# Kernel optimization log

Hardware: AMD Instinct MI355X
Metric: run time of the kernel (lower is better)

The kernel has to match this reference:

```python
import jax, jax.numpy as jnp
import numpy as np

EMBED_DIM = 512
NUM_HEADS = 8
HEAD_DIM = EMBED_DIM // NUM_HEADS
REL_MAX = 16
NUM_POS_IDS = 2 * REL_MAX + 1 + 1  # 34 (directed + padding id)
PADDING_IDX = 0
B, S = 2, 2048


def setup_inputs() -> dict:
    key = jax.random.key(0)
    ks = jax.random.split(key, 9)
    Q = jax.random.normal(ks[0], (B, S, EMBED_DIM), dtype=jnp.float32)
    K = jax.random.normal(ks[1], (B, S, EMBED_DIM), dtype=jnp.float32)
    V = jax.random.normal(ks[2], (B, S, EMBED_DIM), dtype=jnp.float32)
    rel_pos_ids = jax.random.randint(ks[3], (B, S, S), 0, NUM_POS_IDS, dtype=jnp.int64) if jax.config.jax_enable_x64 else jax.random.randint(ks[3], (B, S, S), 0, NUM_POS_IDS, dtype=jnp.int32)
    scale = 0.02
    Wq = jax.random.normal(ks[4], (EMBED_DIM, EMBED_DIM), dtype=jnp.float32) * scale
    Wk = jax.random.normal(ks[5], (EMBED_DIM, EMBED_DIM), dtype=jnp.float32) * scale
    Wv = jax.random.normal(ks[6], (EMBED_DIM, EMBED_DIM), dtype=jnp.float32) * scale
    Wo = jax.random.normal(ks[7], (EMBED_DIM, EMBED_DIM), dtype=jnp.float32) * scale
    rel_emb = jax.random.normal(ks[8], (NUM_POS_IDS, EMBED_DIM), dtype=jnp.float32) * scale
    rel_emb = rel_emb.at[PADDING_IDX].set(0.0)  # nn.Embedding padding_idx row is zero
    return {"Q": Q, "K": K, "V": V, "rel_pos_ids": rel_pos_ids,
            "Wq": Wq, "Wk": Wk, "Wv": Wv, "Wo": Wo, "rel_emb": rel_emb}


def _proj(x, W):
    # Linear (no bias) then strided head split: view(B, S, head_dim, H) -> (B, H, S, head_dim)
    b, s, _ = x.shape
    y = x @ W.T
    return y.reshape(b, s, HEAD_DIM, NUM_HEADS).transpose(0, 3, 1, 2)


def _forward(Q, K, V, rel_pos_ids, Wq, Wk, Wv, Wo, rel_emb):
    b, sq, _ = Q.shape
    Qp = _proj(Q, Wq)  # (B, H, Sq, hd)
    Kp = _proj(K, Wk)  # (B, H, Sk, hd)
    Vp = _proj(V, Wv)  # (B, H, Sk, hd)

    # rel_embeds split per head with the same strided layout: (P, hd, H) -> (H, P, hd)
    R = rel_emb.reshape(NUM_POS_IDS, HEAD_DIM, NUM_HEADS).transpose(2, 0, 1)
    # Q_rel: (B, H, Sq, P)
    Q_rel = jnp.einsum('bhsd,hpd->bhsp', Qp, R)
    # gather per-pair relative bias: (B, H, Sq, Sk)
    rel_shift = jnp.take_along_axis(Q_rel, rel_pos_ids[:, None, :, :], axis=3)
    mask = (rel_pos_ids == PADDING_IDX)[:, None, :, :]
    rel_shift = jnp.where(mask, -jnp.inf, rel_shift)

    energy = (jnp.einsum('bhqd,bhkd->bhqk', Qp, Kp) + rel_shift) / jnp.sqrt(jnp.float32(HEAD_DIM))
    attn = jax.nn.softmax(energy, axis=-1)
    out = jnp.einsum('bhqk,bhkd->bhqd', attn, Vp)  # (B, H, Sq, hd)
    # inverse of strided split: (B, Sq, hd, H) -> flatten last two
    out = out.transpose(0, 2, 3, 1).reshape(b, sq, EMBED_DIM)
    return out @ Wo.T


def reference(Q, K, V, rel_pos_ids, Wq, Wk, Wv, Wo, rel_emb):
    return _forward(Q, K, V, rel_pos_ids, Wq, Wk, Wv, Wo, rel_emb)
```

## Files before the change

kernel.cpp:

```cpp
#include <hip/hip_runtime.h>
#include <cstdint>
#include <cstddef>

#define SEQ   2048
#define BBAT  2
#define EMBED 512
#define NH    8
#define HD    64
#define NPOS  34

typedef __bf16 bf16;
typedef __bf16 bf16x8 __attribute__((ext_vector_type(8)));
typedef float  f32x4  __attribute__((ext_vector_type(4)));
typedef int    int32x4 __attribute__((ext_vector_type(4)));

#define ESCALE 0.1803368801111204f

__device__ __forceinline__ f32x4 mfma16(bf16x8 a, bf16x8 b, f32x4 c){
  return __builtin_amdgcn_mfma_f32_16x16x32_bf16(a, b, c, 0, 0, 0);
}

__device__ __forceinline__ void barrier_lgkm(){
  asm volatile("s_waitcnt lgkmcnt(0)" ::: "memory");
  __builtin_amdgcn_s_barrier();
  __builtin_amdgcn_sched_barrier(0);
}

__global__ __launch_bounds__(256) void k_prep(
    const float* __restrict__ Q, const float* __restrict__ K, const float* __restrict__ V,
    const float* __restrict__ Wq, const float* __restrict__ Wk,
    const float* __restrict__ Wv, const float* __restrict__ Wo,
    const float* __restrict__ RE,
    bf16* __restrict__ Qb, bf16* __restrict__ Kb, bf16* __restrict__ Vb,
    bf16* __restrict__ Wall, bf16* __restrict__ Rb)
{
  const int NCONV = 3*524288;
  const int NW = 196608, NO = 262144;
  int i = blockIdx.x*256 + threadIdx.x;
  if (i < NCONV){
    int tsel = i >> 19, j = i & 524287;
    const float* s = tsel==0 ? Q : (tsel==1 ? K : V);
    bf16* d       = tsel==0 ? Qb : (tsel==1 ? Kb : Vb);
    float4 v = ((const float4*)s)[j];
    union { bf16 e[4]; ushort4 u; } pk;
    pk.e[0]=(bf16)v.x; pk.e[1]=(bf16)v.y; pk.e[2]=(bf16)v.z; pk.e[3]=(bf16)v.w;
    ((ushort4*)d)[j] = pk.u;
  } else {
    int j = i - NCONV;
    if (j < NW){
      int w  = j >> 16;
      int r  = j & 65535;
      int np = r >> 7, c4 = (r & 127) << 2;
      const float* W = (w==0) ? Wq : ((w==1) ? Wk : Wv);
      int src = ((np & 63) << 3) + (np >> 6);
      float4 v = *(const float4*)(W + (size_t)src*512 + c4);
      union { bf16 e[4]; ushort4 u; } pk;
      pk.e[0]=(bf16)v.x; pk.e[1]=(bf16)v.y; pk.e[2]=(bf16)v.z; pk.e[3]=(bf16)v.w;
      *(ushort4*)(Wall + (size_t)w*262144 + (size_t)np*512 + c4) = pk.u;
    } else if (j < NW + NO){
      int jj = j - NW;
      int n = jj >> 9, kp = jj & 511;
      int src = ((kp & 63) << 3) + (kp >> 6);
      Wall[(size_t)3*262144 + (size_t)n*512 + kp] = (bf16)Wo[(size_t)n*512 + src];
    } else {
      int jj = j - NW - NO;
      if (jj < 8*48*64){
        int h  = jj / (48*64);
        int r2 = jj - h*(48*64);
        int p  = r2 >> 6, dd = r2 & 63;
        float v = (p < NPOS) ? RE[(size_t)p*512 + dd*8 + h] : 0.f;
        Rb[jj] = (bf16)v;
      }
    }
  }
}

__global__ __launch_bounds__(256,2) void k_gemm_proj(
    const bf16* __restrict__ Qb, const bf16* __restrict__ Kb, const bf16* __restrict__ Vb,
    const bf16* __restrict__ W,  bf16* __restrict__ Qp, bf16* __restrict__ Kp, bf16* __restrict__ Vt)
{
  const bf16* A  = blockIdx.z==0 ? Qb : (blockIdx.z==1 ? Kb : Vb);
  const bf16* Bw = W + (size_t)blockIdx.z*262144;

  __shared__ __align__(16) bf16 As[128][72];
  __shared__ __align__(16) bf16 Bs[64][72];
  const int t = threadIdx.x;
  const int w = t >> 6, lane = t & 63, l15 = lane & 15, quad = lane >> 4;
  const int wm = (w & 1) * 64, wn = (w >> 1) * 32;
  const int m0 = blockIdx.y * 128, n0 = blockIdx.x * 64;

  f32x4 acc[4][2];
  #pragma unroll
  for (int mt=0; mt<4; ++mt)
    #pragma unroll
    for (int nt=0; nt<2; ++nt) acc[mt][nt] = (f32x4){0.f,0.f,0.f,0.f};

  for (int kt = 0; kt < 512; kt += 64){
    #pragma unroll
    for (int i = 0; i < 4; ++i){
      int lin = t + 256*i;
      int r = lin >> 3, c8 = (lin & 7) << 3;
      *(uint4*)&As[r][c8] = *(const uint4*)(A + (size_t)(m0 + r)*512 + kt + c8);
    }
    #pragma unroll
    for (int i = 0; i < 2; ++i){
      int lin = t + 256*i;
      int r = lin >> 3, c8 = (lin & 7) << 3;
      *(uint4*)&Bs[r][c8] = *(const uint4*)(Bw + (size_t)(n0 + r)*512 + kt + c8);
    }
    __syncthreads();
    #pragma unroll
    for (int ks = 0; ks < 2; ++ks){
      bf16x8 am[4], bn[2];
      #pragma unroll
      for (int x=0;x<4;++x) am[x] = *(const bf16x8*)&As[wm + x*16 + l15][ks*32 + quad*8];
      #pragma unroll
      for (int y=0;y<2;++y) bn[y] = *(const bf16x8*)&Bs[wn + y*16 + l15][ks*32 + quad*8];
      #pragma unroll
      for (int mt=0;mt<4;++mt)
        #pragma unroll
        for (int nt=0;nt<2;++nt)
          acc[mt][nt] = mfma16(am[mt], bn[nt], acc[mt][nt]);
    }
    __syncthreads();
  }

  if (blockIdx.z != 2){
    bf16* C = blockIdx.z==0 ? Qp : Kp;
    const float scl = (blockIdx.z==0) ? ESCALE : 1.0f;
    #pragma unroll
    for (int mt=0;mt<4;++mt)
      #pragma unroll
      for (int r=0;r<4;++r){
        int m = m0 + wm + mt*16 + quad*4 + r;
        #pragma unroll
        for (int nt=0;nt<2;++nt)
          C[(size_t)m*512 + n0 + wn + nt*16 + l15] = (bf16)(acc[mt][nt][r] * scl);
      }
  } else {
    bf16 (*VT)[136] = (bf16(*)[136])As;
    #pragma unroll
    for (int mt=0;mt<4;++mt)
      #pragma unroll
      for (int r=0;r<4;++r){
        int m = wm + mt*16 + quad*4 + r;
        #pragma unroll
        for (int nt=0;nt<2;++nt)
          VT[wn + nt*16 + l15][m] = (bf16)acc[mt][nt][r];
      }
    __syncthreads();
    const int h = blockIdx.x, b = m0 >> 11, s0 = m0 & 2047;
    const int n = t >> 2, c0 = (t & 3) * 32;
    bf16* dst = Vt + ((size_t)((b*NH + h)*HD + n))*SEQ + s0 + c0;
    #pragma unroll
    for (int i = 0; i < 4; ++i)
      *(uint4*)(dst + i*8) = *(const uint4*)&VT[n][c0 + i*8];
  }
}

__global__ __launch_bounds__(256,2) void k_gemm_out(
    const bf16* __restrict__ A, const bf16* __restrict__ Bw, float* __restrict__ C)
{
  __shared__ __align__(16) bf16 As[64][72];
  __shared__ __align__(16) bf16 Bs[64][72];
  const int t = threadIdx.x;
  const int w = t >> 6, lane = t & 63, l15 = lane & 15, quad = lane >> 4;
  const int wm = (w & 1) * 32, wn = (w >> 1) * 32;
  const int m0 = blockIdx.y * 64, n0 = blockIdx.x * 64;

  f32x4 acc[2][2];
  #pragma unroll
  for (int mt=0; mt<2; ++mt)
    #pragma unroll
    for (int nt=0; nt<2; ++nt) acc[mt][nt] = (f32x4){0.f,0.f,0.f,0.f};

  for (int kt = 0; kt < 512; kt += 64){
    #pragma unroll
    for (int i = 0; i < 2; ++i){
      int lin = t + 256*i;
      int r = lin >> 3, c8 = (lin & 7) << 3;
      *(uint4*)&As[r][c8] = *(const uint4*)(A  + (size_t)(m0 + r)*512 + kt + c8);
      *(uint4*)&Bs[r][c8] = *(const uint4*)(Bw + (size_t)(n0 + r)*512 + kt + c8);
    }
    __syncthreads();
    #pragma unroll
    for (int ks = 0; ks < 2; ++ks){
      bf16x8 am[2], bn[2];
      #pragma unroll
      for (int x=0;x<2;++x) am[x] = *(const bf16x8*)&As[wm + x*16 + l15][ks*32 + quad*8];
      #pragma unroll
      for (int y=0;y<2;++y) bn[y] = *(const bf16x8*)&Bs[wn + y*16 + l15][ks*32 + quad*8];
      #pragma unroll
      for (int mt=0;mt<2;++mt)
        #pragma unroll
        for (int nt=0;nt<2;++nt)
          acc[mt][nt] = mfma16(am[mt], bn[nt], acc[mt][nt]);
    }
    __syncthreads();
  }
  #pragma unroll
  for (int mt=0;mt<2;++mt)
    #pragma unroll
    for (int r=0;r<4;++r){
      int m = m0 + wm + mt*16 + quad*4 + r;
      #pragma unroll
      for (int nt=0;nt<2;++nt)
        C[(size_t)m*512 + n0 + wn + nt*16 + l15] = acc[mt][nt][r];
    }
}

__global__ __launch_bounds__(256,2) void k_attn(
    const bf16* __restrict__ Qp, const bf16* __restrict__ Kp,
    const bf16* __restrict__ Vt, const bf16* __restrict__ Rb,
    const int* __restrict__ ids, bf16* __restrict__ Out)
{
  __shared__ __align__(16) bf16 Ks[128][72];
  __shared__ __align__(16) bf16 Vs[64][136];
  __shared__ __align__(16) bf16 Ps[64][136];
  __shared__ float lutT[35][65];
  __shared__ float lsum_s[128];

  const int t = threadIdx.x;
  const int b = blockIdx.z, h = blockIdx.y;
  const int q0 = blockIdx.x * 64;
  const int w = t >> 6, lane = t & 63, l15 = lane & 15, quad = lane >> 4;
  const int qh = w & 1, kh = w >> 1;

  const size_t idb = (size_t)b*SEQ*SEQ;
  const bf16* kbase = Kp + (size_t)b*SEQ*EMBED + h*HD;
  const bf16* vbase = Vt + (size_t)(b*NH + h)*HD*SEQ;

  const int krow = t >> 3, kcol = (t & 7) << 3;
  const int vrow = t >> 4, vcol = (t & 15) << 3;

  uint4 ka0, ka1, ka2, ka3, va0, va1, va2, va3;
  uint4 kb0, kb1, kb2, kb3, vb0, vb1, vb2, vb3;
  ka0 = *(const uint4*)(kbase + (size_t)(krow     )*EMBED + kcol);
  ka1 = *(const uint4*)(kbase + (size_t)(krow + 32)*EMBED + kcol);
  ka2 = *(const uint4*)(kbase + (size_t)(krow + 64)*EMBED + kcol);
  ka3 = *(const uint4*)(kbase + (size_t)(krow + 96)*EMBED + kcol);
  va0 = *(const uint4*)(vbase + (size_t)(vrow     )*SEQ + vcol);
  va1 = *(const uint4*)(vbase + (size_t)(vrow + 16)*SEQ + vcol);
  va2 = *(const uint4*)(vbase + (size_t)(vrow + 32)*SEQ + vcol);
  va3 = *(const uint4*)(vbase + (size_t)(vrow + 48)*SEQ + vcol);

  int32x4 nid[2][4];
  #pragma unroll
  for (int mt=0; mt<2; ++mt)
    #pragma unroll
    for (int nt=0; nt<4; ++nt)
      nid[mt][nt] = *(const int32x4*)(ids + idb
          + (size_t)(q0 + qh*32 + mt*16 + l15)*SEQ
          + kh*64 + nt*16 + quad*4);

  {
    const bf16* qbrow = Qp + (size_t)(b*SEQ + q0 + w*16 + l15)*EMBED + h*HD;
    bf16x8 ab0 = *(const bf16x8*)(qbrow + quad*8);
    bf16x8 ab1 = *(const bf16x8*)(qbrow + 32 + quad*8);
    const bf16* rh = Rb + h*3072;
    #pragma unroll
    for (int nt = 0; nt < 3; ++nt){
      bf16x8 r0 = *(const bf16x8*)(rh + (nt*16 + l15)*64 + quad*8);
      bf16x8 r1 = *(const bf16x8*)(rh + (nt*16 + l15)*64 + 32 + quad*8);
      f32x4 c = (f32x4){0.f,0.f,0.f,0.f};
      c = mfma16(ab0, r0, c);
      c = mfma16(ab1, r1, c);
      int p = nt*16 + l15;
      if (p < NPOS){
        #pragma unroll
        for (int r = 0; r < 4; ++r)
          lutT[p][w*16 + quad*4 + r] = (p == 0) ? -1e30f : c[r];
      }
    }
  }

  bf16x8 bq[2][2];
  #pragma unroll
  for (int mt = 0; mt < 2; ++mt){
    const bf16* qrow = Qp + (size_t)(b*SEQ + q0 + qh*32 + mt*16 + l15)*EMBED + h*HD;
    bq[mt][0] = *(const bf16x8*)(qrow + quad*8);
    bq[mt][1] = *(const bf16x8*)(qrow + 32 + quad*8);
  }

  f32x4 acc[2][4];
  #pragma unroll
  for (int mt=0;mt<2;++mt)
    #pragma unroll
    for (int nt=0;nt<4;++nt) acc[mt][nt] = (f32x4){0.f,0.f,0.f,0.f};
  float lsum[2] = {0.f, 0.f};

#define ATTN_BODY(KT, K0,K1,K2,K3, V0,V1,V2,V3, L0,L1,L2,L3, M0,M1,M2,M3)       \
  {                                                                             \
    barrier_lgkm();              \
    *(uint4*)&Ks[krow     ][kcol] = K0;                                         \
    *(uint4*)&Ks[krow + 32][kcol] = K1;                                         \
    *(uint4*)&Ks[krow + 64][kcol] = K2;                                         \
    *(uint4*)&Ks[krow + 96][kcol] = K3;                                         \
    *(uint4*)&Vs[vrow     ][vcol] = V0;                                         \
    *(uint4*)&Vs[vrow + 16][vcol] = V1;                                         \
    *(uint4*)&Vs[vrow + 32][vcol] = V2;                                         \
    *(uint4*)&Vs[vrow + 48][vcol] = V3;                                         \
    if ((KT) < 15){                                                             \
      const bf16* kp2 = kbase + (size_t)(((KT)+1)*128)*EMBED + kcol;            \
      const bf16* vp2 = vbase + ((KT)+1)*128 + vcol;                            \
      L0 = *(const uint4*)(kp2 + (size_t)(krow     )*EMBED);                    \
      L1 = *(const uint4*)(kp2 + (size_t)(krow + 32)*EMBED);                    \
      L2 = *(const uint4*)(kp2 + (size_t)(krow + 64)*EMBED);                    \
      L3 = *(const uint4*)(kp2 + (size_t)(krow + 96)*EMBED);                    \
      M0 = *(const uint4*)(vp2 + (size_t)(vrow     )*SEQ);                      \
      M1 = *(const uint4*)(vp2 + (size_t)(vrow + 16)*SEQ);                      \
      M2 = *(const uint4*)(vp2 + (size_t)(vrow + 32)*SEQ);                      \
      M3 = *(const uint4*)(vp2 + (size_t)(vrow + 48)*SEQ);                      \
    }                                                                           \
    barrier_lgkm();                \
    float wvv[2][4][4];                                                         \
    _Pragma("unroll")                                                           \
    for (int mt = 0; mt < 2; ++mt){                                             \
      const float* lcol = &lutT[0][qh*32 + mt*16 + l15];                        \
      _Pragma("unroll")                                                         \
      for (int nt = 0; nt < 4; ++nt){                                           \
        int32x4 v = nid[mt][nt];                                                \
        wvv[mt][nt][0] = lcol[v[0] * 65];                                       \
        wvv[mt][nt][1] = lcol[v[1] * 65];                                       \
        wvv[mt][nt][2] = lcol[v[2] * 65];                                       \
        wvv[mt][nt][3] = lcol[v[3] * 65];                                       \
      }                                                                         \
    }                                                                           \
    if ((KT) < 15){                                                             \
      _Pragma("unroll")                                                         \
      for (int mt = 0; mt < 2; ++mt)                                            \
        _Pragma("unroll")                                                       \
        for (int nt = 0; nt < 4; ++nt)                                          \
          nid[mt][nt] = *(const int32x4*)(ids + idb                             \
              + (size_t)(q0 + qh*32 + mt*16 + l15)*SEQ                          \
              + (((KT)+1)*128) + kh*64 + nt*16 + quad*4);                       \
    }                                                                           \
    f32x4 sf[2][4];                                                             \
    __builtin_amdgcn_s_setprio(1);                                              \
    _Pragma("unroll")                                                           \
    for (int nt = 0; nt < 4; ++nt){                                             \
      bf16x8 ak0 = *(const bf16x8*)&Ks[kh*64 + nt*16 + l15][quad*8];            \
      bf16x8 ak1 = *(const bf16x8*)&Ks[kh*64 + nt*16 + l15][32 + quad*8];       \
      _Pragma("unroll")                                                         \
      for (int mt = 0; mt < 2; ++mt){                                           \
        f32x4 c = (f32x4){0.f,0.f,0.f,0.f};                                     \
        c = mfma16(ak0, bq[mt][0], c);                                          \
        c = mfma16(ak1, bq[mt][1], c);                                          \
        sf[mt][nt] = c;                                                         \
      }                                                                         \
    }                                                                           \
    __builtin_amdgcn_s_setprio(0);                                              \
    _Pragma("unroll")                                                           \
    for (int mt = 0; mt < 2; ++mt){                                             \
      _Pragma("unroll")                                                         \
      for (int nt = 0; nt < 4; ++nt){                                           \
        union { bf16 e[4]; uint2 u; } pk;                                       \
        float p0 = __builtin_amdgcn_exp2f(sf[mt][nt][0] + wvv[mt][nt][0]);      \
        float p1 = __builtin_amdgcn_exp2f(sf[mt][nt][1] + wvv[mt][nt][1]);      \
        float p2 = __builtin_amdgcn_exp2f(sf[mt][nt][2] + wvv[mt][nt][2]);      \
        float p3 = __builtin_amdgcn_exp2f(sf[mt][nt][3] + wvv[mt][nt][3]);      \
        pk.e[0] = (bf16)p0; pk.e[1] = (bf16)p1;                                 \
        pk.e[2] = (bf16)p2; pk.e[3] = (bf16)p3;                                 \
        lsum[mt] += (p0 + p1) + (p2 + p3);                                      \
        *(uint2*)&Ps[qh*32 + mt*16 + l15][kh*64 + nt*16 + quad*4] = pk.u;       \
      }                                                                         \
    }                                                                           \
    __builtin_amdgcn_s_setprio(1);                                              \
    _Pragma("unroll")                                                           \
    for (int ks = 0; ks < 2; ++ks){                                             \
      bf16x8 ap[2];                                                             \
      _Pragma("unroll")                                                         \
      for (int mt = 0; mt < 2; ++mt)                                            \
        ap[mt] = *(const bf16x8*)&Ps[qh*32 + mt*16 + l15][kh*64 + ks*32 + quad*8]; \
      _Pragma("unroll")                                                         \
      for (int nt = 0; nt < 4; ++nt){                                           \
        bf16x8 bv = *(const bf16x8*)&Vs[nt*16 + l15][kh*64 + ks*32 + quad*8];   \
        _Pragma("unroll")                                                       \
        for (int mt = 0; mt < 2; ++mt)                                          \
          acc[mt][nt] = mfma16(ap[mt], bv, acc[mt][nt]);                        \
      }                                                                         \
    }                                                                           \
    __builtin_amdgcn_s_setprio(0);                                              \
  }

  for (int kt2 = 0; kt2 < 16; kt2 += 2){
    ATTN_BODY(kt2,     ka0,ka1,ka2,ka3, va0,va1,va2,va3, kb0,kb1,kb2,kb3, vb0,vb1,vb2,vb3)
    ATTN_BODY(kt2 + 1, kb0,kb1,kb2,kb3, vb0,vb1,vb2,vb3, ka0,ka1,ka2,ka3, va0,va1,va2,va3)
  }
#undef ATTN_BODY

  __syncthreads();

  #pragma unroll
  for (int mt = 0; mt < 2; ++mt){
    float v = lsum[mt];
    v += __shfl_xor(v, 16);
    v += __shfl_xor(v, 32);
    if (quad == 0) lsum_s[kh*64 + qh*32 + mt*16 + l15] = v;
  }

  float* xch = (float*)&Ps[0][0];
  if (kh == 1){
    #pragma unroll
    for (int mt = 0; mt < 2; ++mt)
      #pragma unroll
      for (int nt = 0; nt < 4; ++nt){
        f32x4 a = acc[mt][nt];
        #pragma unroll
        for (int r = 0; r < 4; ++r)
          xch[(qh*32 + mt*16 + quad*4 + r)*65 + nt*16 + l15] = a[r];
      }
  }
  __syncthreads();

  if (kh == 0){
    #pragma unroll
    for (int mt = 0; mt < 2; ++mt){
      #pragma unroll
      for (int r = 0; r < 4; ++r){
        int ql = qh*32 + mt*16 + quad*4 + r;
        float inv = __builtin_amdgcn_rcpf(lsum_s[ql] + lsum_s[64 + ql]);
        #pragma unroll
        for (int nt = 0; nt < 4; ++nt){
          float o = acc[mt][nt][r] + xch[ql*65 + nt*16 + l15];
          Out[(size_t)(b*SEQ + q0 + ql)*EMBED + h*HD + nt*16 + l15] = (bf16)(o*inv);
        }
      }
    }
  }
}

extern "C" void kernel_launch(void* const* d_in, const int* in_sizes, int n_in,
                              void* d_out, int out_size, void* d_ws, size_t ws_size,
                              hipStream_t stream)
{
  (void)in_sizes; (void)n_in; (void)out_size;
  const float* Q  = (const float*)d_in[0];
  const float* K  = (const float*)d_in[1];
  const float* V  = (const float*)d_in[2];
  const int*   ID = (const int*)d_in[3];
  const float* Wq = (const float*)d_in[4];
  const float* Wk = (const float*)d_in[5];
  const float* Wv = (const float*)d_in[6];
  const float* Wo = (const float*)d_in[7];
  const float* RE = (const float*)d_in[8];
  float* out = (float*)d_out;

  const size_t MB = (size_t)1 << 20;
  if (ws_size < 36*MB) return;
  char* ws = (char*)d_ws;
  bf16*  Qb    = (bf16*)(ws + 0*MB);
  bf16*  Kb    = (bf16*)(ws + 4*MB);
  bf16*  Vb    = (bf16*)(ws + 8*MB);
  bf16*  Qp    = (bf16*)(ws + 12*MB);
  bf16*  Kp    = (bf16*)(ws + 16*MB);
  bf16*  Vt    = (bf16*)(ws + 20*MB);
  bf16*  Wall  = (bf16*)(ws + 24*MB);
  bf16*  Wop   = Wall + (size_t)3*262144;
  bf16*  Rb    = (bf16*)(ws + 26*MB);
  bf16*  AO    = (bf16*)(ws + 0*MB);

  k_prep      <<<dim3(8032),    256, 0, stream>>>(Q, K, V, Wq, Wk, Wv, Wo, RE,
                                                  Qb, Kb, Vb, Wall, Rb);
  k_gemm_proj <<<dim3(8,32,3),  256, 0, stream>>>(Qb, Kb, Vb, Wall, Qp, Kp, Vt);
  k_attn      <<<dim3(32,8,2),  256, 0, stream>>>(Qp, Kp, Vt, Rb, ID, AO);
  k_gemm_out  <<<dim3(8,64),    256, 0, stream>>>(AO, Wop, out);
}
```

Baseline: 184.1 us.

## Enlarge GEMM tiles to 128x128 and register-prefetch next K tile

Both projection and output GEMMs move to 128x128 block tiles with 4x4 MFMA tiles per wave. Each K step is software-pipelined: the next tile is loaded from global memory into registers while the current tile is computed, and MFMA sections run at raised wave priority. The aim is to hide global load latency and increase reuse per LDS load. The cost is half as many blocks (384 and 128) and higher register pressure, which could hurt occupancy. The V transpose epilogue is adapted to cover two heads per block.

```diff
diff --git a/kernel.cpp b/kernel.cpp
--- a/kernel.cpp
+++ b/kernel.cpp
@@ -75,85 +75,123 @@
   }
 }
 
-__global__ __launch_bounds__(256,2) void k_gemm_proj(
+__global__ __launch_bounds__(256,2) void k_proj(
     const bf16* __restrict__ Qb, const bf16* __restrict__ Kb, const bf16* __restrict__ Vb,
-    const bf16* __restrict__ W,  bf16* __restrict__ Qp, bf16* __restrict__ Kp, bf16* __restrict__ Vt)
+    const bf16* __restrict__ W,
+    bf16* __restrict__ Qp, bf16* __restrict__ Kp, bf16* __restrict__ Vt)
 {
-  const bf16* A  = blockIdx.z==0 ? Qb : (blockIdx.z==1 ? Kb : Vb);
-  const bf16* Bw = W + (size_t)blockIdx.z*262144;
-
-  __shared__ __align__(16) bf16 As[128][72];
-  __shared__ __align__(16) bf16 Bs[64][72];
+  const int z = blockIdx.z;
+  const bf16* A  = z==0 ? Qb : (z==1 ? Kb : Vb);
+  const bf16* Bw = W + (size_t)z*262144;
+
+  __shared__ __align__(16) bf16 AB[2][128][72];
+  bf16 (*As)[72] = AB[0];
+  bf16 (*Bs)[72] = AB[1];
+
   const int t = threadIdx.x;
   const int w = t >> 6, lane = t & 63, l15 = lane & 15, quad = lane >> 4;
-  const int wm = (w & 1) * 64, wn = (w >> 1) * 32;
-  const int m0 = blockIdx.y * 128, n0 = blockIdx.x * 64;
-
-  f32x4 acc[4][2];
+  const int wm = (w & 1) * 64, wn = (w >> 1) * 64;
+  const int m0 = blockIdx.y * 128, n0 = blockIdx.x * 128;
+  const int row = t >> 3, c8 = (t & 7) << 3;
+
+  const bf16* Abase = A  + (size_t)(m0 + row)*512 + c8;
+  const bf16* Bbase = Bw + (size_t)(n0 + row)*512 + c8;
+
+  uint4 pa0,pa1,pa2,pa3, pb0,pb1,pb2,pb3;
+  uint4 qa0,qa1,qa2,qa3, qb0,qb1,qb2,qb3;
+  pa0 = *(const uint4*)(Abase);
+  pa1 = *(const uint4*)(Abase + 32*512);
+  pa2 = *(const uint4*)(Abase + 64*512);
+  pa3 = *(const uint4*)(Abase + 96*512);
+  pb0 = *(const uint4*)(Bbase);
+  pb1 = *(const uint4*)(Bbase + 32*512);
+  pb2 = *(const uint4*)(Bbase + 64*512);
+  pb3 = *(const uint4*)(Bbase + 96*512);
+
+  f32x4 acc[4][4];
   #pragma unroll
   for (int mt=0; mt<4; ++mt)
     #pragma unroll
-    for (int nt=0; nt<2; ++nt) acc[mt][nt] = (f32x4){0.f,0.f,0.f,0.f};
-
-  for (int kt = 0; kt < 512; kt += 64){
-    #pragma unroll
-    for (int i = 0; i < 4; ++i){
-      int lin = t + 256*i;
-      int r = lin >> 3, c8 = (lin & 7) << 3;
-      *(uint4*)&As[r][c8] = *(const uint4*)(A + (size_t)(m0 + r)*512 + kt + c8);
-    }
-    #pragma unroll
-    for (int i = 0; i < 2; ++i){
-      int lin = t + 256*i;
-      int r = lin >> 3, c8 = (lin & 7) << 3;
-      *(uint4*)&Bs[r][c8] = *(const uint4*)(Bw + (size_t)(n0 + r)*512 + kt + c8);
-    }
-    __syncthreads();
-    #pragma unroll
-    for (int ks = 0; ks < 2; ++ks){
-      bf16x8 am[4], bn[2];
-      #pragma unroll
-      for (int x=0;x<4;++x) am[x] = *(const bf16x8*)&As[wm + x*16 + l15][ks*32 + quad*8];
-      #pragma unroll
-      for (int y=0;y<2;++y) bn[y] = *(const bf16x8*)&Bs[wn + y*16 + l15][ks*32 + quad*8];
-      #pragma unroll
-      for (int mt=0;mt<4;++mt)
-        #pragma unroll
-        for (int nt=0;nt<2;++nt)
-          acc[mt][nt] = mfma16(am[mt], bn[nt], acc[mt][nt]);
-    }
-    __syncthreads();
-  }
-
-  if (blockIdx.z != 2){
-    bf16* C = blockIdx.z==0 ? Qp : Kp;
-    const float scl = (blockIdx.z==0) ? ESCALE : 1.0f;
+    for (int nt=0; nt<4; ++nt) acc[mt][nt] = (f32x4){0.f,0.f,0.f,0.f};
+
+#define PROJ_BODY(KT, A0,A1,A2,A3, B0,B1,B2,B3, LA0,LA1,LA2,LA3, LB0,LB1,LB2,LB3) \
+  {                                                                             \
+    barrier_lgkm();                       \
+    *(uint4*)&As[row     ][c8] = A0;                                            \
+    *(uint4*)&As[row + 32][c8] = A1;                                            \
+    *(uint4*)&As[row + 64][c8] = A2;                                            \
+    *(uint4*)&As[row + 96][c8] = A3;                                            \
+    *(uint4*)&Bs[row     ][c8] = B0;                                            \
+    *(uint4*)&Bs[row + 32][c8] = B1;                                            \
+    *(uint4*)&Bs[row + 64][c8] = B2;                                            \
+    *(uint4*)&Bs[row + 96][c8] = B3;                                            \
+    if ((KT) < 7){                                                              \
+      const bf16* ap2 = Abase + ((KT)+1)*64;                                    \
+      const bf16* bp2 = Bbase + ((KT)+1)*64;                                    \
+      LA0 = *(const uint4*)(ap2);                                               \
+      LA1 = *(const uint4*)(ap2 + 32*512);                                      \
+      LA2 = *(const uint4*)(ap2 + 64*512);                                      \
+      LA3 = *(const uint4*)(ap2 + 96*512);                                      \
+      LB0 = *(const uint4*)(bp2);                                               \
+      LB1 = *(const uint4*)(bp2 + 32*512);                                      \
+      LB2 = *(const uint4*)(bp2 + 64*512);                                      \
+      LB3 = *(const uint4*)(bp2 + 96*512);                                      \
+    }                                                                           \
+    barrier_lgkm();                  \
+    __builtin_amdgcn_s_setprio(1);                                              \
+    _Pragma("unroll")                                                           \
+    for (int ks = 0; ks < 2; ++ks){                                             \
+      bf16x8 am[4], bn[4];                                                      \
+      _Pragma("unroll")                                                         \
+      for (int x=0;x<4;++x) am[x] = *(const bf16x8*)&As[wm + x*16 + l15][ks*32 + quad*8]; \
+      _Pragma("unroll")                                                         \
+      for (int y=0;y<4;++y) bn[y] = *(const bf16x8*)&Bs[wn + y*16 + l15][ks*32 + quad*8]; \
+      _Pragma("unroll")                                                         \
+      for (int mt=0;mt<4;++mt)                                                  \
+        _Pragma("unroll")                                                       \
+        for (int nt=0;nt<4;++nt)                                                \
+          acc[mt][nt] = mfma16(am[mt], bn[nt], acc[mt][nt]);                    \
+    }                                                                           \
+    __builtin_amdgcn_s_setprio(0);                                              \
+  }
+
+  for (int kt2 = 0; kt2 < 8; kt2 += 2){
+    PROJ_BODY(kt2,     pa0,pa1,pa2,pa3, pb0,pb1,pb2,pb3, qa0,qa1,qa2,qa3, qb0,qb1,qb2,qb3)
+    PROJ_BODY(kt2 + 1, qa0,qa1,qa2,qa3, qb0,qb1,qb2,qb3, pa0,pa1,pa2,pa3, pb0,pb1,pb2,pb3)
+  }
+#undef PROJ_BODY
+
+  if (z != 2){
+    bf16* C = z==0 ? Qp : Kp;
+    const float scl = (z==0) ? ESCALE : 1.0f;
     #pragma unroll
     for (int mt=0;mt<4;++mt)
       #pragma unroll
       for (int r=0;r<4;++r){
         int m = m0 + wm + mt*16 + quad*4 + r;
         #pragma unroll
-        for (int nt=0;nt<2;++nt)
+        for (int nt=0;nt<4;++nt)
           C[(size_t)m*512 + n0 + wn + nt*16 + l15] = (bf16)(acc[mt][nt][r] * scl);
       }
   } else {
-    bf16 (*VT)[136] = (bf16(*)[136])As;
+    __syncthreads();
+    bf16 (*VT)[136] = (bf16(*)[136])AB;
     #pragma unroll
     for (int mt=0;mt<4;++mt)
       #pragma unroll
       for (int r=0;r<4;++r){
         int m = wm + mt*16 + quad*4 + r;
         #pragma unroll
-        for (int nt=0;nt<2;++nt)
+        for (int nt=0;nt<4;++nt)
           VT[wn + nt*16 + l15][m] = (bf16)acc[mt][nt][r];
       }
     __syncthreads();
-    const int h = blockIdx.x, b = m0 >> 11, s0 = m0 & 2047;
-    const int n = t >> 2, c0 = (t & 3) * 32;
-    bf16* dst = Vt + ((size_t)((b*NH + h)*HD + n))*SEQ + s0 + c0;
-    #pragma unroll
-    for (int i = 0; i < 4; ++i)
+    const int b = m0 >> 11, s0 = m0 & 2047;
+    const int n = t >> 1, c0 = (t & 1) * 64;
+    const int h = blockIdx.x*2 + (n >> 6), d = n & 63;
+    bf16* dst = Vt + ((size_t)((b*NH + h)*HD + d))*SEQ + s0 + c0;
+    #pragma unroll
+    for (int i = 0; i < 8; ++i)
       *(uint4*)(dst + i*8) = *(const uint4*)&VT[n][c0 + i*8];
   }
 }
@@ -161,50 +199,90 @@
 __global__ __launch_bounds__(256,2) void k_gemm_out(
     const bf16* __restrict__ A, const bf16* __restrict__ Bw, float* __restrict__ C)
 {
-  __shared__ __align__(16) bf16 As[64][72];
-  __shared__ __align__(16) bf16 Bs[64][72];
+  __shared__ __align__(16) bf16 AB[2][128][72];
+  bf16 (*As)[72] = AB[0];
+  bf16 (*Bs)[72] = AB[1];
+
   const int t = threadIdx.x;
   const int w = t >> 6, lane = t & 63, l15 = lane & 15, quad = lane >> 4;
-  const int wm = (w & 1) * 32, wn = (w >> 1) * 32;
-  const int m0 = blockIdx.y * 64, n0 = blockIdx.x * 64;
-
-  f32x4 acc[2][2];
-  #pragma unroll
-  for (int mt=0; mt<2; ++mt)
-    #pragma unroll
-    for (int nt=0; nt<2; ++nt) acc[mt][nt] = (f32x4){0.f,0.f,0.f,0.f};
-
-  for (int kt = 0; kt < 512; kt += 64){
-    #pragma unroll
-    for (int i = 0; i < 2; ++i){
-      int lin = t + 256*i;
-      int r = lin >> 3, c8 = (lin & 7) << 3;
-      *(uint4*)&As[r][c8] = *(const uint4*)(A  + (size_t)(m0 + r)*512 + kt + c8);
-      *(uint4*)&Bs[r][c8] = *(const uint4*)(Bw + (size_t)(n0 + r)*512 + kt + c8);
-    }
-    __syncthreads();
-    #pragma unroll
-    for (int ks = 0; ks < 2; ++ks){
-      bf16x8 am[2], bn[2];
-      #pragma unroll
-      for (int x=0;x<2;++x) am[x] = *(const bf16x8*)&As[wm + x*16 + l15][ks*32 + quad*8];
-      #pragma unroll
-      for (int y=0;y<2;++y) bn[y] = *(const bf16x8*)&Bs[wn + y*16 + l15][ks*32 + quad*8];
-      #pragma unroll
-      for (int mt=0;mt<2;++mt)
-        #pragma unroll
-        for (int nt=0;nt<2;++nt)
-          acc[mt][nt] = mfma16(am[mt], bn[nt], acc[mt][nt]);
-    }
-    __syncthreads();
-  }
-  #pragma unroll
-  for (int mt=0;mt<2;++mt)
+  const int wm = (w & 1) * 64, wn = (w >> 1) * 64;
+  const int m0 = blockIdx.y * 128, n0 = blockIdx.x * 128;
+  const int row = t >> 3, c8 = (t & 7) << 3;
+
+  const bf16* Abase = A  + (size_t)(m0 + row)*512 + c8;
+  const bf16* Bbase = Bw + (size_t)(n0 + row)*512 + c8;
+
+  uint4 pa0,pa1,pa2,pa3, pb0,pb1,pb2,pb3;
+  uint4 qa0,qa1,qa2,qa3, qb0,qb1,qb2,qb3;
+  pa0 = *(const uint4*)(Abase);
+  pa1 = *(const uint4*)(Abase + 32*512);
+  pa2 = *(const uint4*)(Abase + 64*512);
+  pa3 = *(const uint4*)(Abase + 96*512);
+  pb0 = *(const uint4*)(Bbase);
+  pb1 = *(const uint4*)(Bbase + 32*512);
+  pb2 = *(const uint4*)(Bbase + 64*512);
+  pb3 = *(const uint4*)(Bbase + 96*512);
+
+  f32x4 acc[4][4];
+  #pragma unroll
+  for (int mt=0; mt<4; ++mt)
+    #pragma unroll
+    for (int nt=0; nt<4; ++nt) acc[mt][nt] = (f32x4){0.f,0.f,0.f,0.f};
+
+#define OUT_BODY(KT, A0,A1,A2,A3, B0,B1,B2,B3, LA0,LA1,LA2,LA3, LB0,LB1,LB2,LB3) \
+  {                                                                             \
+    barrier_lgkm();                                                             \
+    *(uint4*)&As[row     ][c8] = A0;                                            \
+    *(uint4*)&As[row + 32][c8] = A1;                                            \
+    *(uint4*)&As[row + 64][c8] = A2;                                            \
+    *(uint4*)&As[row + 96][c8] = A3;                                            \
+    *(uint4*)&Bs[row     ][c8] = B0;                                            \
+    *(uint4*)&Bs[row + 32][c8] = B1;                                            \
+    *(uint4*)&Bs[row + 64][c8] = B2;                                            \
+    *(uint4*)&Bs[row + 96][c8] = B3;                                            \
+    if ((KT) < 7){                                                              \
+      const bf16* ap2 = Abase + ((KT)+1)*64;                                    \
+      const bf16* bp2 = Bbase + ((KT)+1)*64;                                    \
+      LA0 = *(const uint4*)(ap2);                                               \
+      LA1 = *(const uint4*)(ap2 + 32*512);                                      \
+      LA2 = *(const uint4*)(ap2 + 64*512);                                      \
+      LA3 = *(const uint4*)(ap2 + 96*512);                                      \
+      LB0 = *(const uint4*)(bp2);                                               \
+      LB1 = *(const uint4*)(bp2 + 32*512);                                      \
+      LB2 = *(const uint4*)(bp2 + 64*512);                                      \
+      LB3 = *(const uint4*)(bp2 + 96*512);                                      \
+    }                                                                           \
+    barrier_lgkm();                                                             \
+    __builtin_amdgcn_s_setprio(1);                                              \
+    _Pragma("unroll")                                                           \
+    for (int ks = 0; ks < 2; ++ks){                                             \
+      bf16x8 am[4], bn[4];                                                      \
+      _Pragma("unroll")                                                         \
+      for (int x=0;x<4;++x) am[x] = *(const bf16x8*)&As[wm + x*16 + l15][ks*32 + quad*8]; \
+      _Pragma("unroll")                                                         \
+      for (int y=0;y<4;++y) bn[y] = *(const bf16x8*)&Bs[wn + y*16 + l15][ks*32 + quad*8]; \
+      _Pragma("unroll")                                                         \
+      for (int mt=0;mt<4;++mt)                                                  \
+        _Pragma("unroll")                                                       \
+        for (int nt=0;nt<4;++nt)                                                \
+          acc[mt][nt] = mfma16(am[mt], bn[nt], acc[mt][nt]);                    \
+    }                                                                           \
+    __builtin_amdgcn_s_setprio(0);                                              \
+  }
+
+  for (int kt2 = 0; kt2 < 8; kt2 += 2){
+    OUT_BODY(kt2,     pa0,pa1,pa2,pa3, pb0,pb1,pb2,pb3, qa0,qa1,qa2,qa3, qb0,qb1,qb2,qb3)
+    OUT_BODY(kt2 + 1, qa0,qa1,qa2,qa3, qb0,qb1,qb2,qb3, pa0,pa1,pa2,pa3, pb0,pb1,pb2,pb3)
+  }
+#undef OUT_BODY
+
+  #pragma unroll
+  for (int mt=0;mt<4;++mt)
     #pragma unroll
     for (int r=0;r<4;++r){
       int m = m0 + wm + mt*16 + quad*4 + r;
       #pragma unroll
-      for (int nt=0;nt<2;++nt)
+      for (int nt=0;nt<4;++nt)
         C[(size_t)m*512 + n0 + wn + nt*16 + l15] = acc[mt][nt][r];
     }
 }
@@ -462,7 +540,7 @@
 
   k_prep      <<<dim3(8032),    256, 0, stream>>>(Q, K, V, Wq, Wk, Wv, Wo, RE,
                                                   Qb, Kb, Vb, Wall, Rb);
-  k_gemm_proj <<<dim3(8,32,3),  256, 0, stream>>>(Qb, Kb, Vb, Wall, Qp, Kp, Vt);
+  k_proj      <<<dim3(4,32,3),  256, 0, stream>>>(Qb, Kb, Vb, Wall, Qp, Kp, Vt);
   k_attn      <<<dim3(32,8,2),  256, 0, stream>>>(Qp, Kp, Vt, Rb, ID, AO);
-  k_gemm_out  <<<dim3(8,64),    256, 0, stream>>>(AO, Wop, out);
-}
+  k_gemm_out  <<<dim3(4,32),    256, 0, stream>>>(AO, Wop, out);
+}
```

After: 179.6 us. 2.5% less time.
